# Optimization experiments

Hardware: AMD Instinct MI355X
Metric: run time of the kernel (lower is better)

Reference implementation:

```python
import jax, jax.numpy as jnp
import numpy as np

N = 100000   # nodes
E = 1600000  # edges
IN = 128     # input_dim
H = 64       # hidden_dim
OUT = 2      # output_dim
G = 64       # number of graphs in the batch


def setup_inputs() -> dict:
    key = jax.random.key(0)
    ks = jax.random.split(key, 12)
    x = jax.random.normal(ks[0], (N, IN), dtype=jnp.float32)
    edge_index = jax.random.randint(ks[1], (2, E), 0, N, dtype=jnp.int64)
    batch = jnp.sort(jax.random.randint(ks[2], (N,), 0, G, dtype=jnp.int64))
    s = 0.05
    return {
        "x": x,
        "edge_index": edge_index,
        "batch": batch,
        "W1": jax.random.normal(ks[3], (IN, H), dtype=jnp.float32) * s,
        "b1": jnp.zeros((H,), dtype=jnp.float32),
        "W2": jax.random.normal(ks[4], (H, H), dtype=jnp.float32) * s,
        "b2": jnp.zeros((H,), dtype=jnp.float32),
        "W3": jax.random.normal(ks[5], (H, H), dtype=jnp.float32) * s,
        "b3": jnp.zeros((H,), dtype=jnp.float32),
        "Wm1": jax.random.normal(ks[6], (H, H), dtype=jnp.float32) * s,
        "bm1": jnp.zeros((H,), dtype=jnp.float32),
        "Wm2": jax.random.normal(ks[7], (H, OUT), dtype=jnpp.float32) * s if False else jax.random.normal(ks[7], (H, OUT), dtype=jnp.float32) * s,
        "bm2": jnp.zeros((OUT,), dtype=jnp.float32),
    }


def _gcn_conv(x, W, b, src, dst, norm, n_nodes):
    # PyG GCNConv: h = x @ W; message = norm * h[src]; scatter-add at dst; + bias
    h = x @ W                                  # [N, H]
    msg = h[src] * norm[:, None]               # [E+N, H] gather + scale
    out = jax.ops.segment_sum(msg, dst, num_segments=n_nodes)
    return out + b


def reference(x, edge_index, batch, W1, b1, W2, b2, W3, b3, Wm1, bm1, Wm2, bm2):
    n = x.shape[0]
    # add self-loops (PyG GCNConv default add_self_loops=True)
    loop = jnp.arange(n, dtype=edge_index.dtype)
    src = jnp.concatenate([edge_index[0], loop])
    dst = jnp.concatenate([edge_index[1], loop])
    # symmetric normalization deg^-1/2 (deg over target nodes, incl. self-loops)
    deg = jax.ops.segment_sum(jnp.ones_like(dst, dtype=x.dtype), dst, num_segments=n)
    dinv = jnp.where(deg > 0, jax.lax.rsqrt(deg), 0.0)
    norm = dinv[src] * dinv[dst]               # [E+N]

    h = jax.nn.relu(_gcn_conv(x, W1, b1, src, dst, norm, n))   # dropout: eval -> identity
    h = jax.nn.relu(_gcn_conv(h, W2, b2, src, dst, norm, n))
    h = jax.nn.relu(_gcn_conv(h, W3, b3, src, dst, norm, n))

    # global_mean_pool over batch ids
    sums = jax.ops.segment_sum(h, batch, num_segments=G)       # [G, H]
    cnts = jax.ops.segment_sum(jnp.ones((n,), dtype=h.dtype), batch, num_segments=G)
    pooled = sums / jnp.maximum(cnts, 1.0)[:, None]

    # MLP head: Linear -> ReLU -> (Dropout eval) -> Linear
    z = jax.nn.relu(pooled @ Wm1 + bm1)
    return z @ Wm2 + bm2                                       # [G, OUT]
```

## Files before the change

kernel.cpp:

```cpp
#include <hip/hip_runtime.h>
#include <hip/hip_bf16.h>

#define NNODES 100000
#define NEDGES 1600000
#define IND 128
#define HD 64
#define OUTD 2
#define NG 64
#define BINSHIFT 9
#define BINSZ 512
#define BSTRIDE 12288
#define PB 256

typedef __attribute__((ext_vector_type(8))) short short8v;
typedef __attribute__((ext_vector_type(4))) float floatx4;

static __device__ __forceinline__ unsigned short f2bf(float f) {
    __hip_bfloat16 h = __float2bfloat16(f);
    return *(unsigned short*)&h;
}
static __device__ __forceinline__ float bf2f(unsigned short u) {
    __hip_bfloat16 h = *(__hip_bfloat16*)&u;
    return __bfloat162float(h);
}

__global__ __launch_bounds__(1024) void binP_kernel(const int* __restrict__ src,
                                                    const int* __restrict__ dst,
                                                    int* __restrict__ binCount,
                                                    unsigned int* __restrict__ binned,
                                                    int E, int nbins) {
    __shared__ int lh[256];
    __shared__ int lbase[256];
    int t = threadIdx.x;
    if (t < 256) lh[t] = 0;
    __syncthreads();
    int ebpb = (E + PB - 1) / PB;
    int e0 = blockIdx.x * ebpb;
    int e1 = min(e0 + ebpb, E);
    int dcache[8];
    int ec = 0;
    for (int e = e0 + t; e < e1; e += 1024) {
        int d = dst[e];
        dcache[ec++] = d;
        atomicAdd(&lh[d >> BINSHIFT], 1);
    }
    __syncthreads();
    if (t < nbins) {
        int c = lh[t];
        if (c > 0) lbase[t] = atomicAdd(&binCount[t], c);
        lh[t] = 0;
    }
    __syncthreads();
    ec = 0;
    for (int e = e0 + t; e < e1; e += 1024) {
        int d = dcache[ec++];
        int b = d >> BINSHIFT;
        int idx = atomicAdd(&lh[b], 1);
        binned[(size_t)b * BSTRIDE + lbase[b] + idx] =
            ((unsigned int)(d & (BINSZ - 1)) << 17) | (unsigned int)src[e];
    }
}

__global__ __launch_bounds__(1024) void binHD_kernel(const unsigned int* __restrict__ binned,
                                                     const int* __restrict__ binCount,
                                                     float* __restrict__ dinv,
                                                     unsigned int* __restrict__ rowinfo,
                                                     int* __restrict__ ssrc, int n) {
    __shared__ int dh[BINSZ];
    __shared__ int rp[BINSZ];
    __shared__ int wsum[4];
    int b = blockIdx.x, t = threadIdx.x;
    int lane = t & 63, wv = t >> 6;
    if (t < BINSZ) dh[t] = 0;
    __syncthreads();
    int s0 = b * BSTRIDE;
    int cnt = binCount[b];
    for (int i = t; i < cnt; i += 1024)
        atomicAdd(&dh[binned[s0 + i] >> 17], 1);
    __syncthreads();
    if (t < BINSZ) {
        int node = (b << BINSHIFT) + t;
        if (node < n) dinv[node] = 1.0f / sqrtf((float)(dh[t] + 1));
    }
    int d0 = 0, d1 = 0, p = 0;
    if (t < 256) { d0 = dh[2 * t]; d1 = dh[2 * t + 1]; p = d0 + d1; }
    int sc = p;
#pragma unroll
    for (int d = 1; d < 64; d <<= 1) { int v = __shfl_up(sc, d, 64); if (lane >= d) sc += v; }
    if (t < 256 && lane == 63) wsum[wv] = sc;
    __syncthreads();
    if (t < 256) {
        int add = 0;
        for (int w2 = 0; w2 < wv; w2++) add += wsum[w2];
        int ex = sc - p + add;
        rp[2 * t]     = ex;
        rp[2 * t + 1] = ex + d0;
    }
    __syncthreads();
    if (t < BINSZ) {
        int node = (b << BINSHIFT) + t;
        if (node < n)
            rowinfo[node] = ((unsigned int)(s0 + rp[t]) << 10) |
                            (unsigned int)min(dh[t], 1023);
    }
    __syncthreads();
    for (int i = t; i < cnt; i += 1024) {
        unsigned int rec = binned[s0 + i];
        int doff = rec >> 17;
        int s = rec & 0x1FFFF;
        int idx = atomicSub(&dh[doff], 1) - 1;
        ssrc[s0 + rp[doff] + idx] = s;
    }
}

__global__ __launch_bounds__(256) void prep_kernel(const float* __restrict__ W1,
                                                   const float* __restrict__ W2,
                                                   const float* __restrict__ W3,
                                                   unsigned short* __restrict__ WT1,
                                                   unsigned short* __restrict__ WT2,
                                                   unsigned short* __restrict__ WT3,
                                                   const int* __restrict__ batch,
                                                   float* __restrict__ gcnt, int n) {
    int blk = blockIdx.x;
    if (blk < 64) {
        int i = blk * 256 + threadIdx.x;
        if (i < 64 * IND) {
            int nn2 = i / IND, k = i - nn2 * IND;
            WT1[i] = f2bf(W1[k * 64 + nn2]);
        } else if (i < 64 * IND + 64 * HD) {
            int j = i - 64 * IND;
            int nn2 = j / HD, k = j - nn2 * HD;
            WT2[j] = f2bf(W2[k * 64 + nn2]);
        } else {
            int j = i - 64 * IND - 64 * HD;
            int nn2 = j / HD, k = j - nn2 * HD;
            WT3[j] = f2bf(W3[k * 64 + nn2]);
        }
    } else {
        __shared__ float lg[NG];
        int t = threadIdx.x;
        if (t < NG) lg[t] = 0.f;
        __syncthreads();
        int nb2 = gridDim.x - 64;
        int per = (n + nb2 - 1) / nb2;
        int i0 = (blk - 64) * per;
        int i1 = min(i0 + per, n);
        for (int i = i0 + t; i < i1; i += 256)
            atomicAdd(&lg[batch[i]], 1.f);
        __syncthreads();
        if (t < NG) atomicAdd(&gcnt[t], lg[t]);
    }
}

template <int K, bool BF16IN>
__global__ __launch_bounds__(256) void mm_mfma_kernel(const void* __restrict__ Xv,
                                                      const unsigned short* __restrict__ WT,
                                                      const float* __restrict__ dinv,
                                                      unsigned short* __restrict__ Tb, int nn) {
    const int lane = threadIdx.x & 63;
    const int wv   = threadIdx.x >> 6;
    const int nb   = blockIdx.x * 64 + wv * 16;
    if (nb >= nn) return;
    const int col  = lane & 15;
    const int quad = lane >> 4;
    const int m    = min(nb + col, nn - 1);

    floatx4 acc0 = {0.f, 0.f, 0.f, 0.f};
    floatx4 acc1 = {0.f, 0.f, 0.f, 0.f};
    floatx4 acc2 = {0.f, 0.f, 0.f, 0.f};
    floatx4 acc3 = {0.f, 0.f, 0.f, 0.f};

#pragma unroll
    for (int ks = 0; ks < K; ks += 32) {
        const int k0 = ks + quad * 8;
        short8v a;
        if (BF16IN) {
            a = *(const short8v*)((const unsigned short*)Xv + (size_t)m * K + k0);
        } else {
            const float* xr = (const float*)Xv + (size_t)m * K + k0;
            float4 f0 = *(const float4*)(xr);
            float4 f1 = *(const float4*)(xr + 4);
            a[0] = (short)f2bf(f0.x); a[1] = (short)f2bf(f0.y);
            a[2] = (short)f2bf(f0.z); a[3] = (short)f2bf(f0.w);
            a[4] = (short)f2bf(f1.x); a[5] = (short)f2bf(f1.y);
            a[6] = (short)f2bf(f1.z); a[7] = (short)f2bf(f1.w);
        }
        short8v b0 = *(const short8v*)(WT + (size_t)(0  + col) * K + k0);
        short8v b1 = *(const short8v*)(WT + (size_t)(16 + col) * K + k0);
        short8v b2 = *(const short8v*)(WT + (size_t)(32 + col) * K + k0);
        short8v b3 = *(const short8v*)(WT + (size_t)(48 + col) * K + k0);
        acc0 = __builtin_amdgcn_mfma_f32_16x16x32_bf16(a, b0, acc0, 0, 0, 0);
        acc1 = __builtin_amdgcn_mfma_f32_16x16x32_bf16(a, b1, acc1, 0, 0, 0);
        acc2 = __builtin_amdgcn_mfma_f32_16x16x32_bf16(a, b2, acc2, 0, 0, 0);
        acc3 = __builtin_amdgcn_mfma_f32_16x16x32_bf16(a, b3, acc3, 0, 0, 0);
    }

#pragma unroll
    for (int r = 0; r < 4; r++) {
        int node = nb + quad * 4 + r;
        if (node < nn) {
            float sc = dinv[node];
            unsigned short* o = Tb + (size_t)node * 64 + col;
            o[0]  = f2bf(sc * acc0[r]);
            o[16] = f2bf(sc * acc1[r]);
            o[32] = f2bf(sc * acc2[r]);
            o[48] = f2bf(sc * acc3[r]);
        }
    }
}

__global__ __launch_bounds__(256) void agg_kernel(const unsigned short* __restrict__ Tb,
                                                  const unsigned int* __restrict__ rowinfo,
                                                  const int* __restrict__ ssrc,
                                                  const float* __restrict__ dinv,
                                                  const float* __restrict__ bias,
                                                  unsigned short* __restrict__ Ob, int nn) {
    int wave = __builtin_amdgcn_readfirstlane((blockIdx.x * 256 + threadIdx.x) >> 6);
    int lane = threadIdx.x & 63;
    if (wave >= nn) return;
    int n = wave;
    float acc = bf2f(Tb[(size_t)n * 64 + lane]);
    unsigned int info = rowinfo[n];
    int rb = (int)(info >> 10);
    int re = rb + (int)(info & 1023);
    int i = rb;
    for (; i + 16 <= re; i += 16) {
        int s[16];
#pragma unroll
        for (int k = 0; k < 16; k++) s[k] = ssrc[i + k];
        float v[16];
#pragma unroll
        for (int k = 0; k < 16; k++) v[k] = bf2f(Tb[(size_t)s[k] * 64 + lane]);
#pragma unroll
        for (int k = 0; k < 16; k++) acc += v[k];
    }
    for (; i + 4 <= re; i += 4) {
        int s0 = ssrc[i], s1 = ssrc[i + 1], s2 = ssrc[i + 2], s3 = ssrc[i + 3];
        float v0 = bf2f(Tb[(size_t)s0 * 64 + lane]);
        float v1 = bf2f(Tb[(size_t)s1 * 64 + lane]);
        float v2 = bf2f(Tb[(size_t)s2 * 64 + lane]);
        float v3 = bf2f(Tb[(size_t)s3 * 64 + lane]);
        acc += v0; acc += v1; acc += v2; acc += v3;
    }
    for (; i < re; i++)
        acc += bf2f(Tb[(size_t)ssrc[i] * 64 + lane]);
    float o = dinv[n] * acc + bias[lane];
    o = o > 0.f ? o : 0.f;
    Ob[(size_t)n * 64 + lane] = f2bf(o);
}

__global__ __launch_bounds__(256) void pool_kernel(const unsigned short* __restrict__ Hb,
                                                   const int* __restrict__ batch,
                                                   float* __restrict__ pooled, int nn) {
    int wid = (blockIdx.x * 256 + threadIdx.x) >> 6;
    int lane = threadIdx.x & 63;
    int nwaves = (gridDim.x * 256) >> 6;
    int per = (nn + nwaves - 1) / nwaves;
    int n0 = wid * per;
    int n1 = n0 + per; if (n1 > nn) n1 = nn;
    if (n0 >= n1) return;
    int cur = batch[n0];
    float acc = 0.f;
    for (int n = n0; n < n1; ++n) {
        int g = batch[n];
        if (g != cur) {
            atomicAdd(&pooled[cur * 64 + lane], acc);
            acc = 0.f; cur = g;
        }
        acc += bf2f(Hb[(size_t)n * 64 + lane]);
    }
    atomicAdd(&pooled[cur * 64 + lane], acc);
}

__global__ __launch_bounds__(256) void head_kernel(const float* __restrict__ pooled,
                                                   const float* __restrict__ gcnt,
                                                   const float* __restrict__ Wm1,
                                                   const float* __restrict__ bm1,
                                                   const float* __restrict__ Wm2,
                                                   const float* __restrict__ bm2,
                                                   float* __restrict__ out) {
    __shared__ float P[NG * 64];
    __shared__ float Z[NG * 64];
    int tid = threadIdx.x;
    for (int i = tid; i < NG * 64; i += 256) {
        int g = i >> 6;
        float c = gcnt[g];
        c = c > 1.f ? c : 1.f;
        P[i] = pooled[i] / c;
    }
    __syncthreads();
    for (int i = tid; i < NG * 64; i += 256) {
        int g = i >> 6, j = i & 63;
        float a = bm1[j];
#pragma unroll 8
        for (int k = 0; k < 64; ++k) a += P[g * 64 + k] * Wm1[k * 64 + j];
        Z[i] = a > 0.f ? a : 0.f;
    }
    __syncthreads();
    for (int i = tid; i < NG * OUTD; i += 256) {
        int g = i / OUTD, o = i % OUTD;
        float a = bm2[o];
#pragma unroll 8
        for (int k = 0; k < 64; ++k) a += Z[g * 64 + k] * Wm2[k * OUTD + o];
        out[i] = a;
    }
}

extern "C" void kernel_launch(void* const* d_in, const int* in_sizes, int n_in,
                              void* d_out, int out_size, void* d_ws, size_t ws_size,
                              hipStream_t stream) {
    const float* x    = (const float*)d_in[0];
    const int*  edge  = (const int*)d_in[1];
    const int*  batch = (const int*)d_in[2];
    const float* W1 = (const float*)d_in[3];
    const float* b1 = (const float*)d_in[4];
    const float* W2 = (const float*)d_in[5];
    const float* b2 = (const float*)d_in[6];
    const float* W3 = (const float*)d_in[7];
    const float* b3 = (const float*)d_in[8];
    const float* Wm1 = (const float*)d_in[9];
    const float* bm1 = (const float*)d_in[10];
    const float* Wm2 = (const float*)d_in[11];
    const float* bm2 = (const float*)d_in[12];

    const int N_ = in_sizes[2];
    const int E_ = in_sizes[1] / 2;
    const int* src = edge;
    const int* dst = edge + E_;
    const int nbins = (N_ + BINSZ - 1) >> BINSHIFT;

    char* w = (char*)d_ws;
    auto alloc = [&](size_t bytes) -> void* {
        void* p = (void*)w;
        w += (bytes + 255) & ~(size_t)255;
        return p;
    };
    float* dinv   = (float*)alloc((size_t)N_ * 4);
    unsigned int* rowinfo = (unsigned int*)alloc((size_t)N_ * 4);
    float* pooled = (float*)alloc((size_t)(NG * 64 + NG) * 4);
    int*   binCount = (int*)alloc(256 * 4);
    float* gcnt   = pooled + NG * 64;
    int*   ssrc   = (int*)alloc((size_t)nbins * BSTRIDE * 4);
    unsigned int* binned = (unsigned int*)alloc((size_t)nbins * BSTRIDE * 4);
    unsigned short* Tb  = (unsigned short*)alloc((size_t)N_ * 64 * 2);
    unsigned short* hBb = (unsigned short*)alloc((size_t)N_ * 64 * 2);
    unsigned short* WT1 = (unsigned short*)alloc((size_t)64 * IND * 2);
    unsigned short* WT2 = (unsigned short*)alloc((size_t)64 * HD * 2);
    unsigned short* WT3 = (unsigned short*)alloc((size_t)64 * HD * 2);

    hipMemsetAsync(pooled, 0, (size_t)(NG * 64 + NG) * 4 + 256 * 4 + 256, stream);

    binP_kernel<<<PB, 1024, 0, stream>>>(src, dst, binCount, binned, E_, nbins);
    binHD_kernel<<<nbins, 1024, 0, stream>>>(binned, binCount, dinv, rowinfo, ssrc, N_);

    prep_kernel<<<64 + 16, 256, 0, stream>>>(W1, W2, W3, WT1, WT2, WT3, batch, gcnt, N_);

    const int mmblk = (N_ + 63) / 64;
    const int aggblk = (N_ + 3) / 4;

    mm_mfma_kernel<IND, false><<<mmblk, 256, 0, stream>>>(x, WT1, dinv, Tb, N_);
    agg_kernel<<<aggblk, 256, 0, stream>>>(Tb, rowinfo, ssrc, dinv, b1, hBb, N_);
    mm_mfma_kernel<HD, true><<<mmblk, 256, 0, stream>>>(hBb, WT2, dinv, Tb, N_);
    agg_kernel<<<aggblk, 256, 0, stream>>>(Tb, rowinfo, ssrc, dinv, b2, hBb, N_);
    mm_mfma_kernel<HD, true><<<mmblk, 256, 0, stream>>>(hBb, WT3, dinv, Tb, N_);
    agg_kernel<<<aggblk, 256, 0, stream>>>(Tb, rowinfo, ssrc, dinv, b3, hBb, N_);

    pool_kernel<<<256, 256, 0, stream>>>(hBb, batch, pooled, N_);
    head_kernel<<<1, 256, 0, stream>>>(pooled, gcnt, Wm1, bm1, Wm2, bm2, (float*)d_out);
}
```

Baseline: 383.6 us.

## Vectorize GCN aggregation with 4-edge-parallel quarter-waves and two nodes per wave

The aggregation kernel now handles two nodes per wave. Each 16-lane quarter-wave gathers a different edge's 8-byte (4 bf16) slice, so one wave load covers four neighbour rows at once, and the partial sums are combined with xor shuffles at the end. The edge-list index loads are vectorized as uint4 and prefetched one iteration ahead. To support this, the matmul output layout is permuted so each lane writes 4 contiguous bf16 values, and CSR row starts are padded to multiples of 4 for aligned uint4 index loads. This cuts the number of load instructions and raises memory-level parallelism, at the cost of a cross-lane reduction and more registers.

Measured after the change: 393.3 us. 2.5% more time.

```diff
diff --git a/kernel.cpp b/kernel.cpp
--- a/kernel.cpp
+++ b/kernel.cpp
@@ -22,6 +22,14 @@
 static __device__ __forceinline__ float bf2f(unsigned short u) {
     __hip_bfloat16 h = *(__hip_bfloat16*)&u;
     return __bfloat162float(h);
+}
+
+static __device__ __forceinline__ void unpack_add(uint2 u, float& a0, float& a1,
+                                                  float& a2, float& a3) {
+    a0 += __uint_as_float(u.x << 16);
+    a1 += __uint_as_float(u.x & 0xffff0000u);
+    a2 += __uint_as_float(u.y << 16);
+    a3 += __uint_as_float(u.y & 0xffff0000u);
 }
 
 __global__ __launch_bounds__(1024) void binP_kernel(const int* __restrict__ src,
@@ -83,7 +91,11 @@
         if (node < n) dinv[node] = 1.0f / sqrtf((float)(dh[t] + 1));
     }
     int d0 = 0, d1 = 0, p = 0;
-    if (t < 256) { d0 = dh[2 * t]; d1 = dh[2 * t + 1]; p = d0 + d1; }
+    if (t < 256) {
+        d0 = (dh[2 * t] + 3) & ~3;
+        d1 = (dh[2 * t + 1] + 3) & ~3;
+        p = d0 + d1;
+    }
     int sc = p;
 #pragma unroll
     for (int d = 1; d < 64; d <<= 1) { int v = __shfl_up(sc, d, 64); if (lane >= d) sc += v; }
@@ -185,10 +197,10 @@
             a[4] = (short)f2bf(f1.x); a[5] = (short)f2bf(f1.y);
             a[6] = (short)f2bf(f1.z); a[7] = (short)f2bf(f1.w);
         }
-        short8v b0 = *(const short8v*)(WT + (size_t)(0  + col) * K + k0);
-        short8v b1 = *(const short8v*)(WT + (size_t)(16 + col) * K + k0);
-        short8v b2 = *(const short8v*)(WT + (size_t)(32 + col) * K + k0);
-        short8v b3 = *(const short8v*)(WT + (size_t)(48 + col) * K + k0);
+        short8v b0 = *(const short8v*)(WT + (size_t)(4 * col + 0) * K + k0);
+        short8v b1 = *(const short8v*)(WT + (size_t)(4 * col + 1) * K + k0);
+        short8v b2 = *(const short8v*)(WT + (size_t)(4 * col + 2) * K + k0);
+        short8v b3 = *(const short8v*)(WT + (size_t)(4 * col + 3) * K + k0);
         acc0 = __builtin_amdgcn_mfma_f32_16x16x32_bf16(a, b0, acc0, 0, 0, 0);
         acc1 = __builtin_amdgcn_mfma_f32_16x16x32_bf16(a, b1, acc1, 0, 0, 0);
         acc2 = __builtin_amdgcn_mfma_f32_16x16x32_bf16(a, b2, acc2, 0, 0, 0);
@@ -200,11 +212,12 @@
         int node = nb + quad * 4 + r;
         if (node < nn) {
             float sc = dinv[node];
-            unsigned short* o = Tb + (size_t)node * 64 + col;
-            o[0]  = f2bf(sc * acc0[r]);
-            o[16] = f2bf(sc * acc1[r]);
-            o[32] = f2bf(sc * acc2[r]);
-            o[48] = f2bf(sc * acc3[r]);
+            unsigned int lo = (unsigned int)f2bf(sc * acc0[r]) |
+                              ((unsigned int)f2bf(sc * acc1[r]) << 16);
+            unsigned int hi = (unsigned int)f2bf(sc * acc2[r]) |
+                              ((unsigned int)f2bf(sc * acc3[r]) << 16);
+            uint2 st; st.x = lo; st.y = hi;
+            ((uint2*)Tb)[(size_t)node * 16 + col] = st;
         }
     }
 }
@@ -217,36 +230,125 @@
                                                   unsigned short* __restrict__ Ob, int nn) {
     int wave = __builtin_amdgcn_readfirstlane((blockIdx.x * 256 + threadIdx.x) >> 6);
     int lane = threadIdx.x & 63;
-    if (wave >= nn) return;
-    int n = wave;
-    float acc = bf2f(Tb[(size_t)n * 64 + lane]);
-    unsigned int info = rowinfo[n];
-    int rb = (int)(info >> 10);
-    int re = rb + (int)(info & 1023);
-    int i = rb;
-    for (; i + 16 <= re; i += 16) {
-        int s[16];
-#pragma unroll
-        for (int k = 0; k < 16; k++) s[k] = ssrc[i + k];
-        float v[16];
-#pragma unroll
-        for (int k = 0; k < 16; k++) v[k] = bf2f(Tb[(size_t)s[k] * 64 + lane]);
-#pragma unroll
-        for (int k = 0; k < 16; k++) acc += v[k];
-    }
-    for (; i + 4 <= re; i += 4) {
-        int s0 = ssrc[i], s1 = ssrc[i + 1], s2 = ssrc[i + 2], s3 = ssrc[i + 3];
-        float v0 = bf2f(Tb[(size_t)s0 * 64 + lane]);
-        float v1 = bf2f(Tb[(size_t)s1 * 64 + lane]);
-        float v2 = bf2f(Tb[(size_t)s2 * 64 + lane]);
-        float v3 = bf2f(Tb[(size_t)s3 * 64 + lane]);
-        acc += v0; acc += v1; acc += v2; acc += v3;
-    }
-    for (; i < re; i++)
-        acc += bf2f(Tb[(size_t)ssrc[i] * 64 + lane]);
-    float o = dinv[n] * acc + bias[lane];
-    o = o > 0.f ? o : 0.f;
-    Ob[(size_t)n * 64 + lane] = f2bf(o);
+    int g = lane >> 4;
+    int q = lane & 15;
+    int nA = wave * 2;
+    if (nA >= nn) return;
+    int nB = nA + 1;
+    bool hasB = (nB < nn);
+    const uint2* T64 = (const uint2*)Tb;
+
+    float aA0 = 0.f, aA1 = 0.f, aA2 = 0.f, aA3 = 0.f;
+    float aB0 = 0.f, aB1 = 0.f, aB2 = 0.f, aB3 = 0.f;
+
+    if (g == 0) {
+        uint2 u = T64[(size_t)nA * 16 + q];
+        unpack_add(u, aA0, aA1, aA2, aA3);
+        if (hasB) {
+            uint2 v = T64[(size_t)nB * 16 + q];
+            unpack_add(v, aB0, aB1, aB2, aB3);
+        }
+    }
+
+    unsigned int infoA = rowinfo[nA];
+    unsigned int infoB = hasB ? rowinfo[nB] : 0u;
+    int iA = (int)(infoA >> 10), reA = iA + (int)(infoA & 1023);
+    int iB = (int)(infoB >> 10), reB = iB + (int)(infoB & 1023);
+
+    uint4 sA, sB;
+    bool pA = (iA + 16 <= reA);
+    bool pB = (iB + 16 <= reB);
+    if (pA) sA = *(const uint4*)(ssrc + iA + 4 * g);
+    if (pB) sB = *(const uint4*)(ssrc + iB + 4 * g);
+    while (pA || pB) {
+        uint2 uA0, uA1, uA2, uA3, uB0, uB1, uB2, uB3;
+        if (pA) {
+            uA0 = T64[(size_t)sA.x * 16 + q];
+            uA1 = T64[(size_t)sA.y * 16 + q];
+            uA2 = T64[(size_t)sA.z * 16 + q];
+            uA3 = T64[(size_t)sA.w * 16 + q];
+        }
+        if (pB) {
+            uB0 = T64[(size_t)sB.x * 16 + q];
+            uB1 = T64[(size_t)sB.y * 16 + q];
+            uB2 = T64[(size_t)sB.z * 16 + q];
+            uB3 = T64[(size_t)sB.w * 16 + q];
+        }
+        bool npA = pA && (iA + 32 <= reA);
+        bool npB = pB && (iB + 32 <= reB);
+        uint4 nsA, nsB;
+        if (npA) nsA = *(const uint4*)(ssrc + iA + 16 + 4 * g);
+        if (npB) nsB = *(const uint4*)(ssrc + iB + 16 + 4 * g);
+        if (pA) {
+            unpack_add(uA0, aA0, aA1, aA2, aA3);
+            unpack_add(uA1, aA0, aA1, aA2, aA3);
+            unpack_add(uA2, aA0, aA1, aA2, aA3);
+            unpack_add(uA3, aA0, aA1, aA2, aA3);
+            iA += 16;
+        }
+        if (pB) {
+            unpack_add(uB0, aB0, aB1, aB2, aB3);
+            unpack_add(uB1, aB0, aB1, aB2, aB3);
+            unpack_add(uB2, aB0, aB1, aB2, aB3);
+            unpack_add(uB3, aB0, aB1, aB2, aB3);
+            iB += 16;
+        }
+        sA = nsA; sB = nsB;
+        pA = npA; pB = npB;
+    }
+
+    int eA = iA + g, eB = iB + g;
+    while (eA < reA || eB < reB) {
+        int sa, sb;
+        uint2 ua, ub;
+        if (eA < reA) sa = ssrc[eA];
+        if (eB < reB) sb = ssrc[eB];
+        if (eA < reA) ua = T64[(size_t)sa * 16 + q];
+        if (eB < reB) ub = T64[(size_t)sb * 16 + q];
+        if (eA < reA) { unpack_add(ua, aA0, aA1, aA2, aA3); eA += 4; }
+        if (eB < reB) { unpack_add(ub, aB0, aB1, aB2, aB3); eB += 4; }
+    }
+
+    aA0 += __shfl_xor(aA0, 16, 64); aA0 += __shfl_xor(aA0, 32, 64);
+    aA1 += __shfl_xor(aA1, 16, 64); aA1 += __shfl_xor(aA1, 32, 64);
+    aA2 += __shfl_xor(aA2, 16, 64); aA2 += __shfl_xor(aA2, 32, 64);
+    aA3 += __shfl_xor(aA3, 16, 64); aA3 += __shfl_xor(aA3, 32, 64);
+    aB0 += __shfl_xor(aB0, 16, 64); aB0 += __shfl_xor(aB0, 32, 64);
+    aB1 += __shfl_xor(aB1, 16, 64); aB1 += __shfl_xor(aB1, 32, 64);
+    aB2 += __shfl_xor(aB2, 16, 64); aB2 += __shfl_xor(aB2, 32, 64);
+    aB3 += __shfl_xor(aB3, 16, 64); aB3 += __shfl_xor(aB3, 32, 64);
+
+    if (g == 0) {
+        float4 bv = *(const float4*)(bias + 4 * q);
+        float scA = dinv[nA];
+        float o0 = scA * aA0 + bv.x;
+        float o1 = scA * aA1 + bv.y;
+        float o2 = scA * aA2 + bv.z;
+        float o3 = scA * aA3 + bv.w;
+        o0 = o0 > 0.f ? o0 : 0.f;
+        o1 = o1 > 0.f ? o1 : 0.f;
+        o2 = o2 > 0.f ? o2 : 0.f;
+        o3 = o3 > 0.f ? o3 : 0.f;
+        uint2 st;
+        st.x = (unsigned int)f2bf(o0) | ((unsigned int)f2bf(o1) << 16);
+        st.y = (unsigned int)f2bf(o2) | ((unsigned int)f2bf(o3) << 16);
+        ((uint2*)Ob)[(size_t)nA * 16 + q] = st;
+        if (hasB) {
+            float scB = dinv[nB];
+            float p0 = scB * aB0 + bv.x;
+            float p1 = scB * aB1 + bv.y;
+            float p2 = scB * aB2 + bv.z;
+            float p3 = scB * aB3 + bv.w;
+            p0 = p0 > 0.f ? p0 : 0.f;
+            p1 = p1 > 0.f ? p1 : 0.f;
+            p2 = p2 > 0.f ? p2 : 0.f;
+            p3 = p3 > 0.f ? p3 : 0.f;
+            uint2 sq;
+            sq.x = (unsigned int)f2bf(p0) | ((unsigned int)f2bf(p1) << 16);
+            sq.y = (unsigned int)f2bf(p2) | ((unsigned int)f2bf(p3) << 16);
+            ((uint2*)Ob)[(size_t)nB * 16 + q] = sq;
+        }
+    }
 }
 
 __global__ __launch_bounds__(256) void pool_kernel(const unsigned short* __restrict__ Hb,
@@ -356,7 +458,7 @@
     prep_kernel<<<64 + 16, 256, 0, stream>>>(W1, W2, W3, WT1, WT2, WT3, batch, gcnt, N_);
 
     const int mmblk = (N_ + 63) / 64;
-    const int aggblk = (N_ + 3) / 4;
+    const int aggblk = (N_ + 7) / 8;
 
     mm_mfma_kernel<IND, false><<<mmblk, 256, 0, stream>>>(x, WT1, dinv, Tb, N_);
     agg_kernel<<<aggblk, 256, 0, stream>>>(Tb, rowinfo, ssrc, dinv, b1, hBb, N_);
```
